# Optimization experiments

Hardware: AMD Instinct MI355X
Metric: run time of the kernel (lower is better)

The kernel has to match this reference:

```python
import jax, jax.numpy as jnp
import numpy as np

D_MODEL = 768
N_HEADS = 12
D_K = D_MODEL // N_HEADS
NEG_INF = -1e10


def setup_inputs() -> dict:
    key = jax.random.key(0)
    ks = jax.random.split(key, 12)
    B, S = 2, 4096
    scale = 1.0 / np.sqrt(D_MODEL)
    inp = {
        "q": jax.random.normal(ks[0], (B, S, D_MODEL), jnp.float32),
        "k": jax.random.normal(ks[1], (B, S, D_MODEL), jnp.float32),
        "v": jax.random.normal(ks[2], (B, S, D_MODEL), jnp.float32),
        "mask": jnp.ones((B, S), jnp.int32),
        "Wq": jax.random.normal(ks[3], (D_MODEL, D_MODEL), jnp.float32) * scale,
        "bq": jnp.zeros((D_MODEL,), jnp.float32),
        "Wk": jax.random.normal(ks[4], (D_MODEL, D_MODEL), jnp.float32) * scale,
        "bk": jnp.zeros((D_MODEL,), jnp.float32),
        "Wv": jax.random.normal(ks[5], (D_MODEL, D_MODEL), jnp.float32) * scale,
        "bv": jnp.zeros((D_MODEL,), jnp.float32),
        "Wo": jax.random.normal(ks[6], (D_MODEL, D_MODEL), jnp.float32) * scale,
        "bo": jnp.zeros((D_MODEL,), jnp.float32),
    }
    return inp


def reference(q, k, v, mask, Wq, bq, Wk, bk, Wv, bv, Wo, bo):
    B, Sq, _ = q.shape
    Sk = k.shape[1]
    # linear projections (flax Linear: x @ kernel + bias)
    query = q @ Wq + bq
    key_ = k @ Wk + bk
    value = v @ Wv + bv
    # split heads: [B, H, S, d_k]
    query = query.reshape(B, Sq, N_HEADS, D_K).transpose(0, 2, 1, 3)
    key_ = key_.reshape(B, Sk, N_HEADS, D_K).transpose(0, 2, 1, 3)
    value = value.reshape(B, Sk, N_HEADS, D_K).transpose(0, 2, 1, 3)
    # scores [B, H, Sq, Sk]
    scores = jnp.einsum('bhqd,bhkd->bhqk', query, key_) / jnp.sqrt(
        jnp.asarray(D_K, query.dtype))
    m = mask[:, None, None, :]  # 2D mask -> [B,1,1,Sk]
    scores = jnp.where(m == 0, NEG_INF, scores)
    attn = jax.nn.softmax(scores, axis=-1)
    # dropout deterministic (is_training=False): identity
    x = jnp.einsum('bhqk,bhkd->bhqd', attn, value)
    x = x.transpose(0, 2, 1, 3).reshape(B, Sq, D_MODEL)
    return x @ Wo + bo
```

## Files before the change

### kernel.cpp

```cpp
#include <hip/hip_runtime.h>

typedef __attribute__((ext_vector_type(8))) short short8;
typedef __attribute__((ext_vector_type(4))) float floatx4;
typedef __attribute__((ext_vector_type(16))) float floatx16;
typedef unsigned short ushort_t;

#define S_LEN 4096
#define NH 12
#define DK 64
#define DM 768
#define BQ 128
#define LOG2E 1.4426950408889634f

static __device__ __forceinline__ unsigned short f2bf(float f) {
    unsigned int u = __float_as_uint(f);
    u += 0x7FFFu + ((u >> 16) & 1u);
    return (unsigned short)(u >> 16);
}
static __device__ __forceinline__ unsigned pack2(float a, float b) {
    return (unsigned)f2bf(a) | ((unsigned)f2bf(b) << 16);
}
static __device__ __forceinline__ unsigned pack2f(float a, float b) {
    unsigned au = __float_as_uint(a) + 0x8000u;
    unsigned bu = __float_as_uint(b) + 0x8000u;
    return (bu & 0xFFFF0000u) | (au >> 16);
}
static __device__ __forceinline__ void gld_lds16(const void* g, void* l) {
    __builtin_amdgcn_global_load_lds(
        (__attribute__((address_space(1))) void*)g,
        (__attribute__((address_space(3))) void*)l, 16, 0, 0);
}

__global__ __launch_bounds__(256)
void wtrans_kernel(const float* __restrict__ W0, const float* __restrict__ W1,
                   const float* __restrict__ W2, const float* __restrict__ W3,
                   ushort_t* __restrict__ T0, ushort_t* __restrict__ T1,
                   ushort_t* __restrict__ T2, ushort_t* __restrict__ T3) {
    __shared__ float tile[32][33];
    const int z = blockIdx.z;
    const float* W = (z == 0) ? W0 : (z == 1) ? W1 : (z == 2) ? W2 : W3;
    ushort_t* T = (z == 0) ? T0 : (z == 1) ? T1 : (z == 2) ? T2 : T3;
    const int bx = blockIdx.x, by = blockIdx.y;
    const int tx = threadIdx.x, ty = threadIdx.y;
    #pragma unroll
    for (int j = 0; j < 32; j += 8)
        tile[ty + j][tx] = W[(size_t)(by * 32 + ty + j) * DM + bx * 32 + tx];
    __syncthreads();
    #pragma unroll
    for (int j = 0; j < 32; j += 8)
        T[(size_t)(bx * 32 + ty + j) * DM + by * 32 + tx] = f2bf(tile[tx][ty + j]);
}

__global__ __launch_bounds__(256)
void cvt_kernel(const float* __restrict__ A0, const float* __restrict__ A1,
                const float* __restrict__ A2, ushort_t* __restrict__ O0,
                ushort_t* __restrict__ O1, ushort_t* __restrict__ O2) {
    const int z = blockIdx.y;
    const float* A = (z == 0) ? A0 : (z == 1) ? A1 : A2;
    ushort_t* O = (z == 0) ? O0 : (z == 1) ? O1 : O2;
    const size_t i = ((size_t)blockIdx.x * 256 + threadIdx.x) * 8;
    const float4 f0 = *(const float4*)(A + i);
    const float4 f1 = *(const float4*)(A + i + 4);
    uint4 o;
    o.x = pack2(f0.x, f0.y);
    o.y = pack2(f0.z, f0.w);
    o.z = pack2(f1.x, f1.y);
    o.w = pack2(f1.z, f1.w);
    *(uint4*)(O + i) = o;
}

__global__ __launch_bounds__(256)
void vtrans_kernel(const ushort_t* __restrict__ Vn, ushort_t* __restrict__ Vt) {
    __shared__ ushort_t tl[64 * 72];
    const int s0 = blockIdx.x * 64;
    const size_t bh = blockIdx.y;
    const int t = threadIdx.x;
    {
        const int r = t >> 2, c0 = (t & 3) * 16;
        const uint4* src = (const uint4*)(Vn + (bh * S_LEN + s0 + r) * DK + c0);
        uint4 a0 = src[0], a1 = src[1];
        uint4* dst = (uint4*)&tl[r * 72 + c0];
        dst[0] = a0;
        dst[1] = a1;
    }
    __syncthreads();
    {
        const int d = t >> 2, c0 = (t & 3) * 16;
        alignas(16) ushort_t tmp[16];
        #pragma unroll
        for (int j = 0; j < 16; ++j) tmp[j] = tl[(c0 + j) * 72 + d];
        uint4* dst = (uint4*)(Vt + (bh * DK + d) * S_LEN + s0 + c0);
        dst[0] = *(const uint4*)&tmp[0];
        dst[1] = *(const uint4*)&tmp[8];
    }
}

struct GemmArgs {
    const ushort_t* A[3];
    const ushort_t* Wt[3];
    const float* bias[3];
    void* C[3];
    float scale[3];
};

template <int MODE>
__global__ __launch_bounds__(256, 3)
void gemm_kernel(GemmArgs args) {
    __shared__ ushort_t As[128 * 32];
    __shared__ ushort_t Bs[128 * 32];
    const int z = blockIdx.z;
    const ushort_t* A = args.A[z];
    const ushort_t* Wt = args.Wt[z];
    const float* bias = args.bias[z];
    void* Carg = args.C[z];
    const float scale = args.scale[z];

    const int m0 = blockIdx.x * 128;
    const int n0 = blockIdx.y * 128;
    const int t = threadIdx.x;
    const int w = t >> 6, lane = t & 63, l15 = lane & 15, quad = lane >> 4;
    const int rowoff = (w >> 1) * 64, coloff = (w & 1) * 64;
    const int srow = w * 16 + (lane >> 2);
    const int scol = (lane & 3) * 8;

    floatx4 acc[4][4];
    #pragma unroll
    for (int i = 0; i < 4; ++i)
        #pragma unroll
        for (int j = 0; j < 4; ++j) acc[i][j] = (floatx4){0.f, 0.f, 0.f, 0.f};

    for (int kt = 0; kt < DM; kt += 32) {
        __syncthreads();
        #pragma unroll
        for (int j = 0; j < 2; ++j) {
            const int r = j * 64 + srow;
            gld_lds16(A + (size_t)(m0 + r) * DM + kt + scol, &As[r * 32 + scol]);
            gld_lds16(Wt + (size_t)(n0 + r) * DM + kt + scol, &Bs[r * 32 + scol]);
        }
        __asm__ __volatile__("s_waitcnt vmcnt(0)" ::: "memory");
        __syncthreads();
        short8 af[4], bfr[4];
        #pragma unroll
        for (int i = 0; i < 4; ++i)
            af[i] = *(const short8*)&As[(rowoff + 16 * i + l15) * 32 + quad * 8];
        #pragma unroll
        for (int j = 0; j < 4; ++j)
            bfr[j] = *(const short8*)&Bs[(coloff + 16 * j + l15) * 32 + quad * 8];
        #pragma unroll
        for (int i = 0; i < 4; ++i)
            #pragma unroll
            for (int j = 0; j < 4; ++j)
                acc[i][j] = __builtin_amdgcn_mfma_f32_16x16x32_bf16(af[i], bfr[j], acc[i][j], 0, 0, 0);
    }

    #pragma unroll
    for (int i = 0; i < 4; ++i) {
        #pragma unroll
        for (int j = 0; j < 4; ++j) {
            #pragma unroll
            for (int reg = 0; reg < 4; ++reg) {
                const int m = m0 + rowoff + 16 * i + quad * 4 + reg;
                const int n = n0 + coloff + 16 * j + l15;
                const float v2 = (acc[i][j][reg] + bias[n]) * scale;
                if (MODE == 0) {
                    ushort_t* Out = (ushort_t*)Carg;
                    const int b = m >> 12, s = m & 4095, h = n >> 6, d = n & 63;
                    Out[((size_t)((b * NH + h) * S_LEN + s)) * DK + d] = f2bf(v2);
                } else {
                    float* Out = (float*)Carg;
                    Out[(size_t)m * DM + n] = v2;
                }
            }
        }
    }
}

__global__ __launch_bounds__(256, 3)
void attn_kernel(const ushort_t* __restrict__ Q, const ushort_t* __restrict__ K,
                 const ushort_t* __restrict__ VT, const int* __restrict__ mask,
                 ushort_t* __restrict__ X) {
    __shared__ ushort_t Qs[BQ * DK];
    __shared__ ushort_t Ks0[64 * DK], Ks1[64 * DK];
    __shared__ ushort_t Vs0[64 * DK], Vs1[64 * DK];

    const int id = blockIdx.x;
    const int per = id >> 3;
    const int bh = (id & 7) * 3 + (per >> 5);
    const int qb = per & 31;
    const int b = bh / NH, h = bh - b * NH;
    const size_t bho = (size_t)bh * S_LEN;
    const ushort_t* Vbase = VT + (size_t)bh * DK * S_LEN;
    const int t = threadIdx.x;
    const int w = t >> 6, lane = t & 63, l31 = lane & 31, half = lane >> 5;
    const int q0 = qb * BQ;
    const int swl = l31 & 7;
    const int frow8 = lane >> 3;
    const int fcc = lane & 7;

    auto fillK = [&](int kv0, ushort_t* Kb) {
        #pragma unroll
        for (int j = 0; j < 2; ++j) {
            const int r = (w * 2 + j) * 8 + frow8;
            const int c8 = fcc ^ (r & 7);
            gld_lds16(K + (bho + kv0 + r) * DK + c8 * 8, &Kb[r * DK + fcc * 8]);
        }
    };
    auto fillV = [&](int kv0, ushort_t* Vb) {
        #pragma unroll
        for (int j = 0; j < 2; ++j) {
            const int r = (w * 2 + j) * 8 + frow8;
            const int c8 = fcc ^ (r & 7);
            gld_lds16(Vbase + (size_t)r * S_LEN + kv0 + c8 * 8, &Vb[r * DK + fcc * 8]);
        }
    };

    fillK(0, Ks0);
    fillV(0, Vs0);
    #pragma unroll
    for (int j = 0; j < 4; ++j) {
        const int r = (w * 4 + j) * 8 + frow8;
        const int c8 = fcc ^ (r & 7);
        gld_lds16(Q + (bho + q0 + r) * DK + c8 * 8, &Qs[r * DK + fcc * 8]);
    }
    int ok = 1;
    {
        const int* mrow = mask + (size_t)b * S_LEN + t * 16;
        #pragma unroll
        for (int i = 0; i < 4; ++i) {
            const int4 mm = *(const int4*)(mrow + i * 4);
            ok &= (mm.x != 0) & (mm.y != 0) & (mm.z != 0) & (mm.w != 0);
        }
    }
    const int allones = __syncthreads_and(ok);

    short8 qf[4];
    #pragma unroll
    for (int ks = 0; ks < 4; ++ks) {
        const int c8 = ks * 2 + half;
        qf[ks] = *(const short8*)&Qs[(w * 32 + l31) * DK + ((c8 ^ swl) << 3)];
    }
    ushort_t* Ps = &Qs[(w * 32) * DK];

    floatx16 o[2];
    #pragma unroll
    for (int dt = 0; dt < 2; ++dt)
        #pragma unroll
        for (int r = 0; r < 16; ++r) o[dt][r] = 0.f;
    float l_r = 0.f;

    auto body = [&](int it, const ushort_t* Kc, const ushort_t* Vc,
                    ushort_t* Kn, ushort_t* Vn) {
        __syncthreads();
        if (it + 1 < S_LEN / 64) {
            fillK((it + 1) * 64, Kn);
            fillV((it + 1) * 64, Vn);
        }
        unsigned long long mb = ~0ULL;
        if (!allones) {
            const int mv = mask[(size_t)b * S_LEN + it * 64 + lane];
            mb = __ballot(mv != 0);
        }

        floatx16 st[2];
        #pragma unroll
        for (int kt = 0; kt < 2; ++kt) {
            floatx16 s;
            #pragma unroll
            for (int r = 0; r < 16; ++r) s[r] = 0.f;
            #pragma unroll
            for (int ks = 0; ks < 4; ++ks) {
                const int c8 = ks * 2 + half;
                const short8 kf = *(const short8*)&Kc[(kt * 32 + l31) * DK + ((c8 ^ swl) << 3)];
                s = __builtin_amdgcn_mfma_f32_32x32x16_bf16(kf, qf[ks], s, 0, 0, 0);
            }
            st[kt] = s;
        }

        if (mb != ~0ULL) {
            #pragma unroll
            for (int kt = 0; kt < 2; ++kt) {
                const unsigned bits = (unsigned)(mb >> (kt * 32));
                const unsigned vbits = bits >> (half * 4);
                #pragma unroll
                for (int r = 0; r < 16; ++r)
                    if (!((vbits >> ((r & 3) + 8 * (r >> 2))) & 1)) st[kt][r] = -3.0e10f;
            }
        }

        #pragma unroll
        for (int kt = 0; kt < 2; ++kt) {
            #pragma unroll
            for (int g = 0; g < 4; ++g) {
                const float p0 = __builtin_amdgcn_exp2f(st[kt][g * 4 + 0]);
                const float p1 = __builtin_amdgcn_exp2f(st[kt][g * 4 + 1]);
                const float p2 = __builtin_amdgcn_exp2f(st[kt][g * 4 + 2]);
                const float p3 = __builtin_amdgcn_exp2f(st[kt][g * 4 + 3]);
                l_r += (p0 + p1) + (p2 + p3);
                const int c8 = kt * 4 + g;
                uint2 pk;
                pk.x = pack2f(p0, p1);
                pk.y = pack2f(p2, p3);
                *(uint2*)&Ps[l31 * DK + ((c8 ^ swl) << 3) + half * 4] = pk;
            }
        }
        __asm__ __volatile__("" ::: "memory");

        short8 pf[4];
        #pragma unroll
        for (int ks = 0; ks < 4; ++ks) {
            const int c8 = ks * 2 + half;
            pf[ks] = *(const short8*)&Ps[l31 * DK + ((c8 ^ swl) << 3)];
        }
        #pragma unroll
        for (int dt = 0; dt < 2; ++dt) {
            #pragma unroll
            for (int ks = 0; ks < 4; ++ks) {
                const int c8 = ks * 2 + half;
                const short8 vf = *(const short8*)&Vc[(dt * 32 + l31) * DK + ((c8 ^ swl) << 3)];
                o[dt] = __builtin_amdgcn_mfma_f32_32x32x16_bf16(pf[ks], vf, o[dt], 0, 0, 0);
            }
        }
    };

    for (int it = 0; it < S_LEN / 64; it += 2) {
        body(it, Ks0, Vs0, Ks1, Vs1);
        body(it + 1, Ks1, Vs1, Ks0, Vs0);
    }

    l_r += __shfl_xor(l_r, 32);
    const float inv = 1.0f / l_r;
    float iv[16];
    #pragma unroll
    for (int r = 0; r < 16; ++r)
        iv[r] = __shfl(inv, (r & 3) + 8 * (r >> 2) + 4 * half);
    #pragma unroll
    for (int dt = 0; dt < 2; ++dt)
        #pragma unroll
        for (int r = 0; r < 16; ++r) {
            const int qrow = (r & 3) + 8 * (r >> 2) + 4 * half;
            const int s = q0 + w * 32 + qrow;
            const int d = h * DK + dt * 32 + l31;
            X[((size_t)b * S_LEN + s) * DM + d] = f2bf(o[dt][r] * iv[r]);
        }
}

extern "C" void kernel_launch(void* const* d_in, const int* in_sizes, int n_in,
                              void* d_out, int out_size, void* d_ws, size_t ws_size,
                              hipStream_t stream) {
    const float* q = (const float*)d_in[0];
    const float* k = (const float*)d_in[1];
    const float* v = (const float*)d_in[2];
    const int* mask = (const int*)d_in[3];
    const float* Wq = (const float*)d_in[4];
    const float* bq = (const float*)d_in[5];
    const float* Wk = (const float*)d_in[6];
    const float* bk = (const float*)d_in[7];
    const float* Wv = (const float*)d_in[8];
    const float* bv = (const float*)d_in[9];
    const float* Wo = (const float*)d_in[10];
    const float* bo = (const float*)d_in[11];
    float* out = (float*)d_out;

    const size_t ME = (size_t)2 * S_LEN * DM;
    const size_t WE = (size_t)DM * DM;
    ushort_t* Qb = (ushort_t*)d_ws;
    ushort_t* Kb = Qb + ME;
    ushort_t* Vb = Kb + ME;
    ushort_t* VTb = Vb + ME;
    ushort_t* Xb = VTb + ME;
    ushort_t* Wqt = Xb + ME;
    ushort_t* Wkt = Wqt + WE;
    ushort_t* Wvt = Wkt + WE;
    ushort_t* Wot = Wvt + WE;
    ushort_t* Qa = Xb;
    ushort_t* Ka = VTb;
    ushort_t* Va = (ushort_t*)d_out;

    wtrans_kernel<<<dim3(DM / 32, DM / 32, 4), dim3(32, 8), 0, stream>>>(
        Wq, Wk, Wv, Wo, Wqt, Wkt, Wvt, Wot);

    cvt_kernel<<<dim3((int)(ME / 8 / 256), 3), 256, 0, stream>>>(q, k, v, Qa, Ka, Va);

    GemmArgs g1;
    g1.A[0] = Qa;  g1.A[1] = Ka;  g1.A[2] = Va;
    g1.Wt[0] = Wqt; g1.Wt[1] = Wkt; g1.Wt[2] = Wvt;
    g1.bias[0] = bq; g1.bias[1] = bk; g1.bias[2] = bv;
    g1.C[0] = Qb;  g1.C[1] = Kb;  g1.C[2] = Vb;
    g1.scale[0] = 0.125f * LOG2E;
    g1.scale[1] = 1.0f; g1.scale[2] = 1.0f;
    gemm_kernel<0><<<dim3((2 * S_LEN) / 128, DM / 128, 3), 256, 0, stream>>>(g1);

    vtrans_kernel<<<dim3(S_LEN / 64, 2 * NH), 256, 0, stream>>>(Vb, VTb);

    attn_kernel<<<dim3(768), 256, 0, stream>>>(Qb, Kb, VTb, mask, Xb);

    GemmArgs g2;
    g2.A[0] = Xb;  g2.A[1] = Xb;  g2.A[2] = Xb;
    g2.Wt[0] = Wot; g2.Wt[1] = Wot; g2.Wt[2] = Wot;
    g2.bias[0] = bo; g2.bias[1] = bo; g2.bias[2] = bo;
    g2.C[0] = out; g2.C[1] = out; g2.C[2] = out;
    g2.scale[0] = 1.0f; g2.scale[1] = 1.0f; g2.scale[2] = 1.0f;
    gemm_kernel<1><<<dim3((2 * S_LEN) / 128, DM / 128, 1), 256, 0, stream>>>(g2);
}
```

Baseline: 353.2 us.

## Build P operand in registers via cvt_pk_bf16 and permlane32 swap, add MFMA priority

Replaces the LDS round-trip for the softmax probability tile with an in-register transform. Probabilities are packed to bf16 with the hardware v_cvt_pk_bf16_f32 instruction and redistributed across lane halves with v_permlane32_swap to form the A operand of the PV MFMA. This removes LDS stores and loads and the rounding arithmetic from the inner loop. It also raises wave priority around the MFMA blocks with s_setprio so matrix work is favoured over other waves' VALU work. Correctness depends on the permlane mapping matching the old LDS layout.

```diff
diff --git a/kernel.cpp b/kernel.cpp
--- a/kernel.cpp
+++ b/kernel.cpp
@@ -19,11 +19,6 @@
 }
 static __device__ __forceinline__ unsigned pack2(float a, float b) {
     return (unsigned)f2bf(a) | ((unsigned)f2bf(b) << 16);
-}
-static __device__ __forceinline__ unsigned pack2f(float a, float b) {
-    unsigned au = __float_as_uint(a) + 0x8000u;
-    unsigned bu = __float_as_uint(b) + 0x8000u;
-    return (bu & 0xFFFF0000u) | (au >> 16);
 }
 static __device__ __forceinline__ void gld_lds16(const void* g, void* l) {
     __builtin_amdgcn_global_load_lds(
@@ -239,7 +234,6 @@
         const int c8 = ks * 2 + half;
         qf[ks] = *(const short8*)&Qs[(w * 32 + l31) * DK + ((c8 ^ swl) << 3)];
     }
-    ushort_t* Ps = &Qs[(w * 32) * DK];
 
     floatx16 o[2];
     #pragma unroll
@@ -262,6 +256,7 @@
         }
 
         floatx16 st[2];
+        __builtin_amdgcn_s_setprio(1);
         #pragma unroll
         for (int kt = 0; kt < 2; ++kt) {
             floatx16 s;
@@ -275,6 +270,7 @@
             }
             st[kt] = s;
         }
+        __builtin_amdgcn_s_setprio(0);
 
         if (mb != ~0ULL) {
             #pragma unroll
@@ -287,30 +283,35 @@
             }
         }
 
+        short8 pf[4];
         #pragma unroll
         for (int kt = 0; kt < 2; ++kt) {
+            float p[16];
+            #pragma unroll
+            for (int r = 0; r < 16; ++r) p[r] = __builtin_amdgcn_exp2f(st[kt][r]);
+            #pragma unroll
+            for (int g = 0; g < 4; ++g)
+                l_r += (p[4 * g + 0] + p[4 * g + 1]) + (p[4 * g + 2] + p[4 * g + 3]);
+            unsigned c0[4], c1[4];
             #pragma unroll
             for (int g = 0; g < 4; ++g) {
-                const float p0 = __builtin_amdgcn_exp2f(st[kt][g * 4 + 0]);
-                const float p1 = __builtin_amdgcn_exp2f(st[kt][g * 4 + 1]);
-                const float p2 = __builtin_amdgcn_exp2f(st[kt][g * 4 + 2]);
-                const float p3 = __builtin_amdgcn_exp2f(st[kt][g * 4 + 3]);
-                l_r += (p0 + p1) + (p2 + p3);
-                const int c8 = kt * 4 + g;
-                uint2 pk;
-                pk.x = pack2f(p0, p1);
-                pk.y = pack2f(p2, p3);
-                *(uint2*)&Ps[l31 * DK + ((c8 ^ swl) << 3) + half * 4] = pk;
+                asm("v_cvt_pk_bf16_f32 %0, %1, %2"
+                    : "=v"(c0[g]) : "v"(p[4 * g + 0]), "v"(p[4 * g + 1]));
+                asm("v_cvt_pk_bf16_f32 %0, %1, %2"
+                    : "=v"(c1[g]) : "v"(p[4 * g + 2]), "v"(p[4 * g + 3]));
             }
-        }
-        __asm__ __volatile__("" ::: "memory");
-
-        short8 pf[4];
-        #pragma unroll
-        for (int ks = 0; ks < 4; ++ks) {
-            const int c8 = ks * 2 + half;
-            pf[ks] = *(const short8*)&Ps[l31 * DK + ((c8 ^ swl) << 3)];
-        }
+            asm("v_permlane32_swap_b32 %0, %1" : "+v"(c0[0]), "+v"(c0[1]));
+            asm("v_permlane32_swap_b32 %0, %1" : "+v"(c1[0]), "+v"(c1[1]));
+            asm("v_permlane32_swap_b32 %0, %1" : "+v"(c0[2]), "+v"(c0[3]));
+            asm("v_permlane32_swap_b32 %0, %1" : "+v"(c1[2]), "+v"(c1[3]));
+            union { short8 s8; unsigned u[4]; } w0, w1;
+            w0.u[0] = c0[0]; w0.u[1] = c1[0]; w0.u[2] = c0[1]; w0.u[3] = c1[1];
+            w1.u[0] = c0[2]; w1.u[1] = c1[2]; w1.u[2] = c0[3]; w1.u[3] = c1[3];
+            pf[kt * 2 + 0] = w0.s8;
+            pf[kt * 2 + 1] = w1.s8;
+        }
+
+        __builtin_amdgcn_s_setprio(1);
         #pragma unroll
         for (int dt = 0; dt < 2; ++dt) {
             #pragma unroll
@@ -320,6 +321,7 @@
                 o[dt] = __builtin_amdgcn_mfma_f32_32x32x16_bf16(pf[ks], vf, o[dt], 0, 0, 0);
             }
         }
+        __builtin_amdgcn_s_setprio(0);
     };
 
     for (int it = 0; it < S_LEN / 64; it += 2) {
```

Result: faster. 321.8 us (-8.9%).
